# Performance work log

Measured on AMD Instinct MI355X. Metric: run time of the kernel, lower is better.

The kernel has to match this reference:

```python
import jax, jax.numpy as jnp
import numpy as np

B, N, DIM = 8, 1024, 768
HEADS, HEAD_DIM = 8, 96
EXPERTS, TASKS = 24, 9
SCALE = HEAD_DIM ** -0.5
SWITCHLOSS_W, ZLOSS_W = 0.1, 0.001


def setup_inputs() -> dict:
    key = jax.random.key(0)
    ks = jax.random.split(key, 6)
    x = jax.random.normal(ks[0], (B, N, DIM), jnp.float32)
    Wg = jax.random.normal(ks[1], (TASKS, DIM, EXPERTS), jnp.float32) * 0.02  # per-task gate
    W1 = jax.random.normal(ks[2], (EXPERTS, DIM, HEAD_DIM), jnp.float32) * 0.02  # experts (map)
    W2 = jax.random.normal(ks[3], (EXPERTS, HEAD_DIM, DIM), jnp.float32) * 0.02  # output_experts (reduce)
    Wkv = jax.random.normal(ks[4], (DIM, 2 * HEAD_DIM), jnp.float32) * 0.02      # shared kv proj
    b_kv = jax.random.normal(ks[5], (2 * HEAD_DIM,), jnp.float32) * 0.02
    return {"x": x, "Wg\u200b".replace("\u200b", ""): Wg, "W1": W1, "W2": W2, "Wkv": Wkv, "b_kv": b_kv, "task_bh": 3}


def reference(x, Wg, W1, W2, Wkv, b_kv, task_bh):
    # ---- TaskMoE top-k gating (eval mode: clean logits, no noise/sampling) ----
    logits = jnp.einsum('bnd,de->bne', x, Wg[task_bh])            # [B,N,E]
    probs = jax.nn.softmax(logits, axis=-1)
    top_g, top_i = jax.lax.top_k(probs, HEADS)                    # [B,N,H]
    denom = jax.lax.stop_gradient(jnp.sum(top_g, -1, keepdims=True) + 1e-6)
    gates = top_g / denom                                         # normalized top-k gates

    # ---- aux losses: switch (load-balance) + z-loss (cvloss weight is 0) ----
    me = probs.reshape(-1, EXPERTS).sum(0)
    me = me / me.sum()
    freqs = jnp.zeros((EXPERTS,), x.dtype).at[top_i.reshape(-1)].add(1.0)
    fe = freqs / freqs.sum()
    switch_loss = EXPERTS * jnp.sum(me * fe)
    z_loss = jnp.mean(jax.nn.logsumexp(logits.reshape(-1, EXPERTS), axis=-1) ** 2)
    aux_loss = SWITCHLOSS_W * switch_loss + ZLOSS_W * z_loss

    # ---- MoE map: per-head q from selected experts (dense compute + gather) ----
    all_q = jnp.einsum('bnd,edh->bneh', x, W1)                    # [B,N,E,Hd]
    q = jnp.take_along_axis(all_q, top_i[..., None], axis=2)      # [B,N,H,Hd]

    # ---- shared-KV multi-head attention ----
    kv = x @ Wkv + b_kv
    k, v = jnp.split(kv, 2, axis=-1)                              # [B,N,Hd] each
    attn = jnp.einsum('bihd,bjd->bhij', q, k) * SCALE             # [B,H,N,N]
    attn = jax.nn.softmax(attn, axis=-1)
    o = jnp.einsum('bhij,bjd->bihd', attn, v)                     # [B,N,H,Hd]

    # ---- MoE reduce: gate-weighted combine through output experts ----
    comb = jax.nn.one_hot(top_i, EXPERTS, dtype=x.dtype) * gates[..., None]  # [B,N,H,E]
    mixed = jnp.einsum('bnhe,bnhd->bned', comb, o)                # [B,N,E,Hd]
    out = jnp.einsum('bned,edc->bnc', mixed, W2)                  # [B,N,DIM]
    return out, aux_loss
```

## Files before the change

kernel.cpp:

```cpp
#include <hip/hip_runtime.h>
#include <hip/hip_bf16.h>
#include <stdint.h>

#define DEVFN static __device__ __forceinline__

typedef __attribute__((ext_vector_type(8))) short bf16x8;
typedef __attribute__((ext_vector_type(4))) short s16x4;
typedef __attribute__((ext_vector_type(4))) float f32x4;

static constexpr int TOK = 8192;
static constexpr int DIM = 768;
static constexpr int HEADS = 8;
static constexpr int HD = 96;
static constexpr int EXPERTS = 24;
static constexpr int NQ = 2304;
static constexpr int NQP = 2560;
static constexpr float C2 = 0.14724484f;
static constexpr float THRRAW = 78.0f;

static constexpr size_t OFF_XB   = 0;
static constexpr size_t OFF_BT1  = 12582912;
static constexpr size_t OFF_W2T  = 16515072;
static constexpr size_t OFF_K    = 20054016;
static constexpr size_t OFF_VT   = 21626880;
static constexpr size_t OFF_GATE = 23199744;
static constexpr size_t OFF_TOPI = 23461888;
static constexpr size_t OFF_AUX  = 23724032;
static constexpr size_t OFF_ALLQ = 23724288;
static constexpr size_t OFF_PART = OFF_ALLQ;
static constexpr size_t OFF_LOGT = OFF_ALLQ + 6291456;

DEVFN short f2bf(float f){
  __hip_bfloat16 h = __float2bfloat16(f);
  return __builtin_bit_cast(short, h);
}
DEVFN float bf2f(short u){
  return __bfloat162float(__builtin_bit_cast(__hip_bfloat16, u));
}

DEVFN void gload16(const void* g, void* l){
  auto gp = reinterpret_cast<__attribute__((address_space(1))) unsigned int*>(
      reinterpret_cast<uintptr_t>(g));
  auto lp = reinterpret_cast<__attribute__((address_space(3))) unsigned int*>(
      reinterpret_cast<uintptr_t>(l));
  __builtin_amdgcn_global_load_lds(gp, lp, 16, 0, 0);
}

__global__ __launch_bounds__(256) void prep_kernel(const float* __restrict__ W1,
                                                   const float* __restrict__ Wkv,
                                                   const float* __restrict__ W2,
                                                   short* __restrict__ Bt1,
                                                   short* __restrict__ W2t){
  int bid = blockIdx.x, tid = threadIdx.x;
  if (bid < 6912){
    int i = bid*256 + tid;
    int e = i / (DIM*HD);
    int rem = i - e*(DIM*HD);
    int d = rem / HD, hh = rem - d*HD;
    Bt1[(size_t)(e*HD + hh)*DIM + d] = f2bf(W1[i]);
  } else if (bid < 7488){
    int i = (bid-6912)*256 + tid;
    int d = i / 192, j = i - d*192;
    Bt1[(size_t)(NQ + j)*DIM + d] = f2bf(Wkv[i]);
  } else if (bid < 7680){
    int i = (bid-7488)*256 + tid;
    Bt1[(size_t)(NQ + 192)*DIM + i] = 0;
  } else {
    int i = (bid-7680)*256 + tid;
    int e = i / (HD*DIM);
    int rem = i - e*(HD*DIM);
    int hh = rem / DIM, c = rem - hh*DIM;
    W2t[(size_t)c*NQ + e*HD + hh] = f2bf(W2[i]);
  }
}

__global__ __launch_bounds__(64) void gating_partial(const float* __restrict__ x,
                                                     const float* __restrict__ Wg,
                                                     const int* __restrict__ task,
                                                     short* __restrict__ xb,
                                                     float* __restrict__ partial){
  __shared__ float xl[64*101];
  int lane = threadIdx.x;
  int tg = blockIdx.x >> 3, kc = blockIdx.x & 7;
  int tok0 = tg*64, kbase = kc*96;
  const float* Wt = Wg + (size_t)task[0]*(DIM*EXPERTS) + (size_t)kbase*EXPERTS;

#pragma unroll
  for (int i = 0; i < 24; ++i){
    int c = i*64 + lane;
    int t = c / 24, cc = c - t*24;
    size_t gidx = (size_t)(tok0+t)*DIM + kbase + cc*4;
    float4 v = *reinterpret_cast<const float4*>(x + gidx);
    float* dst = &xl[t*101 + cc*4];
    dst[0] = v.x; dst[1] = v.y; dst[2] = v.z; dst[3] = v.w;
    s16x4 o4;
    o4[0] = f2bf(v.x); o4[1] = f2bf(v.y); o4[2] = f2bf(v.z); o4[3] = f2bf(v.w);
    *reinterpret_cast<s16x4*>(xb + gidx) = o4;
  }
  __syncthreads();

  float acc[EXPERTS];
#pragma unroll
  for (int e = 0; e < EXPERTS; ++e) acc[e] = 0.f;
  for (int d = 0; d < 96; ++d){
    float xv = xl[lane*101 + d];
    const float* wr = Wt + d*EXPERTS;
#pragma unroll
    for (int e = 0; e < EXPERTS; ++e) acc[e] = fmaf(xv, wr[e], acc[e]);
  }
#pragma unroll
  for (int e = 0; e < EXPERTS; ++e)
    partial[(size_t)(kc*EXPERTS + e)*TOK + tok0 + lane] = acc[e];
}

__global__ __launch_bounds__(256) void gating_combine(const float* __restrict__ partial,
                                                      float* __restrict__ logT){
  int idx = blockIdx.x*256 + threadIdx.x;
  float s = 0.f;
#pragma unroll
  for (int kc = 0; kc < 8; ++kc)
    s += partial[(size_t)kc*EXPERTS*TOK + idx];
  logT[idx] = s;
}

__global__ __launch_bounds__(256) void gating_select(const float* __restrict__ logT,
                                                     int* __restrict__ topi,
                                                     float* __restrict__ gates,
                                                     float* __restrict__ auxbuf){
  __shared__ float lme[EXPERTS];
  __shared__ float lfr[EXPERTS];
  __shared__ float lz;
  int tid = threadIdx.x;
  int lane = tid & 63;
  int token = blockIdx.x*256 + tid;
  if (tid < EXPERTS){ lme[tid] = 0.f; lfr[tid] = 0.f; }
  if (tid == 0) lz = 0.f;
  __syncthreads();

  float acc[EXPERTS];
#pragma unroll
  for (int e = 0; e < EXPERTS; ++e)
    acc[e] = logT[(size_t)e*TOK + token];

  float mx = acc[0];
#pragma unroll
  for (int e = 1; e < EXPERTS; ++e) mx = fmaxf(mx, acc[e]);
  unsigned selm = 0; int sel[8]; float sg[8];
#pragma unroll
  for (int t = 0; t < 8; ++t){
    float best = -3.0e38f; int bi = 0;
#pragma unroll
    for (int e = 0; e < EXPERTS; ++e){
      bool ok = !((selm>>e)&1u) && (acc[e] > best);
      best = ok ? acc[e] : best;
      bi   = ok ? e      : bi;
    }
    selm |= (1u<<bi); sel[t] = bi; sg[t] = best;
  }

  float p[EXPERTS]; float S = 0.f;
#pragma unroll
  for (int e = 0; e < EXPERTS; ++e){ p[e] = __expf(acc[e] - mx); S += p[e]; }
  float lse = mx + __logf(S);
  float Sinv = 1.f/S;
  float gsum = 0.f; float pg[8];
#pragma unroll
  for (int t = 0; t < 8; ++t){ pg[t] = __expf(sg[t] - mx)*Sinv; gsum += pg[t]; }
  float dinv = 1.f/(gsum + 1e-6f);

#pragma unroll
  for (int t = 0; t < 8; ++t){
    topi[token*HEADS + t]  = sel[t];
    gates[token*HEADS + t] = pg[t]*dinv;
  }

  float z2 = lse*lse;
#pragma unroll
  for (int d = 1; d < 64; d <<= 1) z2 += __shfl_xor(z2, d, 64);
#pragma unroll
  for (int e = 0; e < EXPERTS; ++e){
    float v = p[e]*Sinv;
#pragma unroll
    for (int d = 1; d < 64; d <<= 1) v += __shfl_xor(v, d, 64);
    bool hit = (sel[0]==e)|(sel[1]==e)|(sel[2]==e)|(sel[3]==e)|
               (sel[4]==e)|(sel[5]==e)|(sel[6]==e)|(sel[7]==e);
    unsigned long long bal = __ballot(hit);
    if (lane == 0){
      atomicAdd(&lme[e], v);
      atomicAdd(&lfr[e], (float)__popcll(bal));
    }
  }
  if (lane == 0) atomicAdd(&lz, z2);
  __syncthreads();
  if (tid < EXPERTS){
    atomicAdd(&auxbuf[tid], lme[tid]);
    atomicAdd(&auxbuf[EXPERTS + tid], lfr[tid]);
  } else if (tid == 63) atomicAdd(&auxbuf[2*EXPERTS], lz);
}

__global__ void aux_final(const float* __restrict__ auxbuf, float* __restrict__ outa){
  if (threadIdx.x != 0 || blockIdx.x != 0) return;
  float ms = 0.f, fs = 0.f;
  for (int e=0;e<EXPERTS;++e){ ms += auxbuf[e]; fs += auxbuf[EXPERTS+e]; }
  float sw = 0.f;
  for (int e=0;e<EXPERTS;++e) sw += (auxbuf[e]/ms)*(auxbuf[EXPERTS+e]/fs);
  sw *= (float)EXPERTS;
  float z = auxbuf[2*EXPERTS] / (float)TOK;
  outa[0] = 0.1f*sw + 0.001f*z;
}

template<bool OUT_BF16>
__global__ __launch_bounds__(256) void gemm_bt(const short* __restrict__ A,
                                               const short* __restrict__ Bt,
                                               void* __restrict__ Cout,
                                               int M, int N, int K){
  __shared__ short As[128*64];
  __shared__ short Bs[128*64];
  int nwg = gridDim.x*gridDim.y;
  int orig = blockIdx.y*gridDim.x + blockIdx.x;
  int cpx = nwg >> 3;
  int swz = (orig & 7)*cpx + (orig >> 3);
  int bx = swz % gridDim.x, by = swz / gridDim.x;

  int tid = threadIdx.x;
  int lane = tid & 63, w = tid >> 6;
  int wr = w >> 1, wc = w & 1;
  int l15 = lane & 15, lg = lane >> 4;
  int m0 = by * 128, n0 = bx * 128;

  f32x4 acc[4][4] = {};

  for (int k0 = 0; k0 < K; k0 += 64){
#pragma unroll
    for (int it = 0; it < 4; ++it){
      int c = it*256 + tid;
      int row = c >> 3, cc = c & 7;
      int csrc = cc ^ (row & 7);
      gload16(A  + (size_t)(m0+row)*K + k0 + csrc*8, (char*)As + (size_t)c*16);
      gload16(Bt + (size_t)(n0+row)*K + k0 + csrc*8, (char*)Bs + (size_t)c*16);
    }
    __syncthreads();
#pragma unroll
    for (int kk = 0; kk < 2; ++kk){
      bf16x8 af[4], bfr[4];
      int jp = (kk*4 + lg) ^ (l15 & 7);
#pragma unroll
      for (int m = 0; m < 4; ++m)
        af[m] = *reinterpret_cast<const bf16x8*>(&As[(wr*64 + m*16 + l15)*64 + jp*8]);
#pragma unroll
      for (int n = 0; n < 4; ++n)
        bfr[n] = *reinterpret_cast<const bf16x8*>(&Bs[(wc*64 + n*16 + l15)*64 + jp*8]);
#pragma unroll
      for (int m = 0; m < 4; ++m)
#pragma unroll
        for (int n = 0; n < 4; ++n)
          acc[m][n] = __builtin_amdgcn_mfma_f32_16x16x32_bf16(af[m], bfr[n], acc[m][n], 0, 0, 0);
    }
    __syncthreads();
  }
#pragma unroll
  for (int m = 0; m < 4; ++m)
#pragma unroll
    for (int n = 0; n < 4; ++n){
      int rbase = m0 + wr*64 + m*16 + lg*4;
      int col   = n0 + wc*64 + n*16 + l15;
#pragma unroll
      for (int r = 0; r < 4; ++r){
        float v = acc[m][n][r];
        size_t idx = (size_t)(rbase + r)*N + col;
        if constexpr (OUT_BF16) ((short*)Cout)[idx] = f2bf(v);
        else                    ((float*)Cout)[idx] = v;
      }
    }
}

__global__ __launch_bounds__(256) void gemm2_fused(const short* __restrict__ o,
                                                   const int* __restrict__ topi,
                                                   const short* __restrict__ W2t,
                                                   float* __restrict__ out){
  __shared__ short As[2][128*64];
  __shared__ short Bs[2][64*64];
  __shared__ signed char hmap[128][24];
  int nwg = gridDim.x*gridDim.y;
  int orig = blockIdx.y*gridDim.x + blockIdx.x;
  int cpx = nwg >> 3;
  int swz = (orig & 7)*cpx + (orig >> 3);
  int bx = swz % gridDim.x, by = swz / gridDim.x;

  int tid = threadIdx.x;
  int lane = tid & 63, w = tid >> 6;
  int l15 = lane & 15, lg = lane >> 4;
  int m0 = by * 128, n0 = bx * 64;

  int* hm32 = (int*)&hmap[0][0];
  for (int i = tid; i < 768; i += 256) hm32[i] = -1;
  __syncthreads();
  for (int i = tid; i < 128*8; i += 256){
    int row = i >> 3, hh = i & 7;
    int e = topi[(size_t)(m0+row)*HEADS + hh];
    hmap[row][e] = (signed char)hh;
  }
  __syncthreads();

  int arow[4], accv[4];
  size_t arbase[4];
#pragma unroll
  for (int it = 0; it < 4; ++it){
    int c = it*256 + tid;
    arow[it] = c >> 3; accv[it] = c & 7;
    arbase[it] = (size_t)(m0 + arow[it])*DIM;
  }

  f32x4 acc[2][4] = {};
  bf16x8 areg[4];

#define STAGE_A(kt, dst)                                                     \
  {                                                                          \
    _Pragma("unroll")                                                        \
    for (int it = 0; it < 4; ++it){                                          \
      unsigned kc = (unsigned)((kt)*8 + accv[it]);                           \
      unsigned e = kc / 12u;                                                 \
      unsigned dc = kc - e*12u;                                              \
      int hh = hmap[arow[it]][e];                                            \
      bf16x8 av = {};                                                        \
      if (hh >= 0)                                                           \
        av = *reinterpret_cast<const bf16x8*>(o + arbase[it] + hh*HD + dc*8);\
      dst[it] = av;                                                          \
    }                                                                        \
  }
#define WRITE_A(buf, src)                                                    \
  {                                                                          \
    _Pragma("unroll")                                                        \
    for (int it = 0; it < 4; ++it)                                           \
      *reinterpret_cast<bf16x8*>(                                            \
        &As[buf][arow[it]*64 + ((accv[it] ^ (arow[it] & 7)))*8]) = src[it];  \
  }
#define STAGE_B(kt, buf)                                                     \
  {                                                                          \
    _Pragma("unroll")                                                        \
    for (int it = 0; it < 2; ++it){                                          \
      int c = it*256 + tid;                                                  \
      int row = c >> 3, cc = c & 7;                                          \
      int csrc = cc ^ (row & 7);                                             \
      gload16(W2t + (size_t)(n0+row)*NQ + (kt)*64 + csrc*8,                  \
              (char*)&Bs[buf][0] + (size_t)c*16);                            \
    }                                                                        \
  }

  STAGE_A(0, areg);
  STAGE_B(0, 0);
  WRITE_A(0, areg);
  __syncthreads();

  for (int kt = 0; kt < 36; ++kt){
    int buf = kt & 1;
    bf16x8 anext[4];
    if (kt < 35){
      STAGE_A(kt+1, anext);
      STAGE_B(kt+1, buf^1);
    }
#pragma unroll
    for (int kk = 0; kk < 2; ++kk){
      int jp = (kk*4 + lg) ^ (l15 & 7);
      bf16x8 af[2], bfr[4];
#pragma unroll
      for (int m = 0; m < 2; ++m)
        af[m] = *reinterpret_cast<const bf16x8*>(&As[buf][(w*32 + m*16 + l15)*64 + jp*8]);
#pragma unroll
      for (int n = 0; n < 4; ++n)
        bfr[n] = *reinterpret_cast<const bf16x8*>(&Bs[buf][(n*16 + l15)*64 + jp*8]);
#pragma unroll
      for (int m = 0; m < 2; ++m)
#pragma unroll
        for (int n = 0; n < 4; ++n)
          acc[m][n] = __builtin_amdgcn_mfma_f32_16x16x32_bf16(af[m], bfr[n], acc[m][n], 0, 0, 0);
    }
    if (kt < 35) WRITE_A(buf^1, anext);
    __syncthreads();
  }
#undef STAGE_A
#undef WRITE_A
#undef STAGE_B

#pragma unroll
  for (int m = 0; m < 2; ++m)
#pragma unroll
    for (int n = 0; n < 4; ++n){
      int rbase = m0 + w*32 + m*16 + lg*4;
      int col   = n0 + n*16 + l15;
#pragma unroll
      for (int r = 0; r < 4; ++r)
        out[(size_t)(rbase + r)*DIM + col] = acc[m][n][r];
    }
}

__global__ __launch_bounds__(256) void split_kv_tile(const short* __restrict__ allq,
                                                     const float* __restrict__ bkv,
                                                     short* __restrict__ Kp,
                                                     short* __restrict__ Vp){
  __shared__ short kv[64*192];
  int bt = blockIdx.x;
  int b = bt >> 4;
  int tid = threadIdx.x;
#pragma unroll
  for (int it = 0; it < 6; ++it){
    int c = it*256 + tid;
    int j = c / 24, cc = c - j*24;
    int token = b*1024 + (bt & 15)*64 + j;
    gload16(allq + (size_t)token*NQP + NQ + cc*8, (char*)kv + (size_t)c*16);
  }
  __syncthreads();
#pragma unroll
  for (int it = 0; it < 3; ++it){
    int c = it*256 + tid;
    int kc = c >> 6, j = c & 63;
    bf16x8 v = *reinterpret_cast<const bf16x8*>(&kv[j*192 + kc*8]);
    bf16x8 o8;
#pragma unroll
    for (int e = 0; e < 8; ++e) o8[e] = f2bf(bf2f(v[e]) + bkv[kc*8 + e]);
    *reinterpret_cast<bf16x8*>(Kp + ((size_t)bt*768 + c)*8) = o8;
  }
#pragma unroll
  for (int it = 0; it < 3; ++it){
    int c = it*256 + tid;
    int kc = c / 96, hd = c - kc*96;
    float bias = bkv[96 + hd];
    bf16x8 o8;
#pragma unroll
    for (int e = 0; e < 8; ++e) o8[e] = f2bf(bf2f(kv[(kc*8 + e)*192 + 96 + hd]) + bias);
    *reinterpret_cast<bf16x8*>(Vp + ((size_t)bt*768 + c)*8) = o8;
  }
}

__global__ __launch_bounds__(256, 2) void attn_fwd(const short* __restrict__ allq,
                                                   const int* __restrict__ topi,
                                                   const float* __restrict__ gates,
                                                   const short* __restrict__ Kp,
                                                   const short* __restrict__ Vp,
                                                   short* __restrict__ o){
  __shared__ short Klds[2][768*8];
  __shared__ short Vlds[2][768*8];
  __shared__ short Plds[4][16*72];
  int qt = blockIdx.x, bh = blockIdx.y;
  int b = bh >> 3, h = bh & 7;
  int tid = threadIdx.x;
  int lane = tid & 63, w = tid >> 6;
  int l15 = lane & 15, lg = lane >> 4;

  bf16x8 qf[2][3];
  int tok0 = b*1024 + qt*128 + w*32;
#pragma unroll
  for (int qm = 0; qm < 2; ++qm){
    int token = tok0 + qm*16 + l15;
    int qe = topi[token*HEADS + h];
    const short* qp = allq + (size_t)token*NQP + qe*HD;
#pragma unroll
    for (int t = 0; t < 3; ++t)
      qf[qm][t] = *reinterpret_cast<const bf16x8*>(qp + t*32 + lg*8);
  }

  f32x4 Oacc[2][6] = {};
  float mrun[2][4], lrun[2][4];
#pragma unroll
  for (int qm = 0; qm < 2; ++qm)
#pragma unroll
    for (int r = 0; r < 4; ++r){ mrun[qm][r] = -1.0e30f; lrun[qm][r] = 0.f; }

  const short* kb = Kp + (size_t)b*16*768*8;
  const short* vb = Vp + (size_t)b*16*768*8;

#pragma unroll
  for (int it = 0; it < 3; ++it){
    int c = it*256 + tid;
    gload16(kb + (size_t)c*8, (char*)&Klds[0][0] + (size_t)c*16);
    gload16(vb + (size_t)c*8, (char*)&Vlds[0][0] + (size_t)c*16);
  }
  __syncthreads();

  int cur = 0;
  for (int nt = 0; nt < 16; ++nt){
    if (nt < 15){
      const short* kn = kb + (size_t)(nt+1)*768*8;
      const short* vn = vb + (size_t)(nt+1)*768*8;
#pragma unroll
      for (int it = 0; it < 3; ++it){
        int c = it*256 + tid;
        gload16(kn + (size_t)c*8, (char*)&Klds[cur^1][0] + (size_t)c*16);
        gload16(vn + (size_t)c*8, (char*)&Vlds[cur^1][0] + (size_t)c*16);
      }
    }

    f32x4 sa[2][4];
    __builtin_amdgcn_s_setprio(1);
#pragma unroll
    for (int ct = 0; ct < 4; ++ct){
      bf16x8 kf[3];
#pragma unroll
      for (int t = 0; t < 3; ++t)
        kf[t] = *reinterpret_cast<const bf16x8*>(&Klds[cur][((t*4+lg)*64 + ct*16 + l15)*8]);
#pragma unroll
      for (int qm = 0; qm < 2; ++qm){
        f32x4 a = {};
#pragma unroll
        for (int t = 0; t < 3; ++t)
          a = __builtin_amdgcn_mfma_f32_16x16x32_bf16(qf[qm][t], kf[t], a, 0, 0, 0);
        sa[qm][ct] = a;
      }
    }
    __builtin_amdgcn_s_setprio(0);

    float pmax[2][4];
    bool need = false;
#pragma unroll
    for (int qm = 0; qm < 2; ++qm)
#pragma unroll
      for (int r = 0; r < 4; ++r){
        pmax[qm][r] = fmaxf(fmaxf(sa[qm][0][r], sa[qm][1][r]),
                            fmaxf(sa[qm][2][r], sa[qm][3][r]));
        need = need || (pmax[qm][r] > mrun[qm][r] + THRRAW);
      }
    if (__any(need)){
#pragma unroll
      for (int qm = 0; qm < 2; ++qm)
#pragma unroll
        for (int r = 0; r < 4; ++r){
          float mx = pmax[qm][r];
#pragma unroll
          for (int d = 1; d < 16; d <<= 1) mx = fmaxf(mx, __shfl_xor(mx, d, 64));
          float mnew = fmaxf(mrun[qm][r], mx);
          float al = exp2f((mrun[qm][r] - mnew)*C2);
          lrun[qm][r] *= al;
#pragma unroll
          for (int dt = 0; dt < 6; ++dt) Oacc[qm][dt][r] *= al;
          mrun[qm][r] = mnew;
        }
    }

#pragma unroll
    for (int qm = 0; qm < 2; ++qm)
#pragma unroll
      for (int r = 0; r < 4; ++r){
        float mc = mrun[qm][r]*C2;
        float s = 0.f;
#pragma unroll
        for (int ct = 0; ct < 4; ++ct){
          float p = exp2f(fmaf(sa[qm][ct][r], C2, -mc));
          sa[qm][ct][r] = p; s += p;
        }
        lrun[qm][r] += s;
      }

    bf16x8 vf[2][6];
#pragma unroll
    for (int ct = 0; ct < 4; ++ct)
#pragma unroll
      for (int r = 0; r < 4; ++r)
        Plds[w][(lg*4 + r)*72 + ct*16 + l15] = f2bf(sa[0][ct][r]);
    __builtin_amdgcn_s_setprio(1);
#pragma unroll
    for (int ks = 0; ks < 2; ++ks){
      bf16x8 pa = *reinterpret_cast<const bf16x8*>(&Plds[w][l15*72 + ks*32 + lg*8]);
#pragma unroll
      for (int dt = 0; dt < 6; ++dt){
        vf[ks][dt] = *reinterpret_cast<const bf16x8*>(&Vlds[cur][((ks*4+lg)*96 + dt*16 + l15)*8]);
        Oacc[0][dt] = __builtin_amdgcn_mfma_f32_16x16x32_bf16(pa, vf[ks][dt], Oacc[0][dt], 0, 0, 0);
      }
    }
    __builtin_amdgcn_s_setprio(0);
#pragma unroll
    for (int ct = 0; ct < 4; ++ct)
#pragma unroll
      for (int r = 0; r < 4; ++r)
        Plds[w][(lg*4 + r)*72 + ct*16 + l15] = f2bf(sa[1][ct][r]);
    __builtin_amdgcn_s_setprio(1);
#pragma unroll
    for (int ks = 0; ks < 2; ++ks){
      bf16x8 pa = *reinterpret_cast<const bf16x8*>(&Plds[w][l15*72 + ks*32 + lg*8]);
#pragma unroll
      for (int dt = 0; dt < 6; ++dt)
        Oacc[1][dt] = __builtin_amdgcn_mfma_f32_16x16x32_bf16(pa, vf[ks][dt], Oacc[1][dt], 0, 0, 0);
    }
    __builtin_amdgcn_s_setprio(0);

    __syncthreads();
    cur ^= 1;
  }

#pragma unroll
  for (int qm = 0; qm < 2; ++qm)
#pragma unroll
    for (int r = 0; r < 4; ++r){
      float l = lrun[qm][r];
#pragma unroll
      for (int d = 1; d < 16; d <<= 1) l += __shfl_xor(l, d, 64);
      int token = tok0 + qm*16 + lg*4 + r;
      float inv = gates[token*HEADS + h] / l;
#pragma unroll
      for (int dt = 0; dt < 6; ++dt)
        o[(size_t)token*DIM + h*HD + dt*16 + l15] = f2bf(Oacc[qm][dt][r]*inv);
    }
}

extern "C" void kernel_launch(void* const* d_in, const int* in_sizes, int n_in,
                              void* d_out, int out_size, void* d_ws, size_t ws_size,
                              hipStream_t stream) {
  (void)in_sizes; (void)n_in; (void)out_size; (void)ws_size;
  const float* x    = (const float*)d_in[0];
  const float* Wg   = (const float*)d_in[1];
  const float* W1   = (const float*)d_in[2];
  const float* W2   = (const float*)d_in[3];
  const float* Wkv  = (const float*)d_in[4];
  const float* bkv  = (const float*)d_in[5];
  const int*   task = (const int*)d_in[6];

  char* ws = (char*)d_ws;
  short* xb    = (short*)(ws + OFF_XB);
  short* o     = (short*)(ws + OFF_XB);
  short* Bt1   = (short*)(ws + OFF_BT1);
  short* W2t   = (short*)(ws + OFF_W2T);
  short* Kp    = (short*)(ws + OFF_K);
  short* Vp    = (short*)(ws + OFF_VT);
  float* gates = (float*)(ws + OFF_GATE);
  int*   topi  = (int*)(ws + OFF_TOPI);
  float* aux   = (float*)(ws + OFF_AUX);
  short* allq  = (short*)(ws + OFF_ALLQ);
  float* part  = (float*)(ws + OFF_PART);
  float* logT  = (float*)(ws + OFF_LOGT);
  float* out   = (float*)d_out;

  hipMemsetAsync(aux, 0, 256, stream);
  prep_kernel   <<<14592, 256, 0, stream>>>(W1, Wkv, W2, Bt1, W2t);
  gating_partial<<<1024, 64, 0, stream>>>(x, Wg, task, xb, part);
  gating_combine<<<768, 256, 0, stream>>>(part, logT);
  gating_select <<<32, 256, 0, stream>>>(logT, topi, gates, aux);
  aux_final     <<<1, 64, 0, stream>>>(aux, out + (size_t)TOK*DIM);
  gemm_bt<true><<<dim3(NQP/128, TOK/128), 256, 0, stream>>>(xb, Bt1, allq, TOK, NQP, DIM);
  split_kv_tile<<<128, 256, 0, stream>>>(allq, bkv, Kp, Vp);
  attn_fwd     <<<dim3(8, 64), 256, 0, stream>>>(allq, topi, gates, Kp, Vp, o);
  gemm2_fused  <<<dim3(DIM/64, TOK/128), 256, 0, stream>>>(o, topi, W2t, out);
}
```

Measured before the change: 203.9 us.

## Tile weight transposes through LDS and split gating reduction into more chunks

```diff
diff --git a/kernel.cpp b/kernel.cpp
--- a/kernel.cpp
+++ b/kernel.cpp
@@ -28,7 +28,7 @@
 static constexpr size_t OFF_AUX  = 23724032;
 static constexpr size_t OFF_ALLQ = 23724288;
 static constexpr size_t OFF_PART = OFF_ALLQ;
-static constexpr size_t OFF_LOGT = OFF_ALLQ + 6291456;
+static constexpr size_t OFF_LOGT = OFF_ALLQ + 12582912;
 
 DEVFN short f2bf(float f){
   __hip_bfloat16 h = __float2bfloat16(f);
@@ -51,26 +51,79 @@
                                                    const float* __restrict__ W2,
                                                    short* __restrict__ Bt1,
                                                    short* __restrict__ W2t){
+  __shared__ float tl[6240];
   int bid = blockIdx.x, tid = threadIdx.x;
-  if (bid < 6912){
-    int i = bid*256 + tid;
-    int e = i / (DIM*HD);
-    int rem = i - e*(DIM*HD);
-    int d = rem / HD, hh = rem - d*HD;
-    Bt1[(size_t)(e*HD + hh)*DIM + d] = f2bf(W1[i]);
-  } else if (bid < 7488){
-    int i = (bid-6912)*256 + tid;
-    int d = i / 192, j = i - d*192;
-    Bt1[(size_t)(NQ + j)*DIM + d] = f2bf(Wkv[i]);
-  } else if (bid < 7680){
-    int i = (bid-7488)*256 + tid;
+
+  if (bid < 288){
+    int e = bid / 12, dt = bid - e*12;
+    int d0 = dt*64;
+    const float* src = W1 + (size_t)e*(DIM*HD);
+#pragma unroll
+    for (int it = 0; it < 6; ++it){
+      int c = it*256 + tid;
+      int row = c / 24, q = c - row*24;
+      float4 v = *reinterpret_cast<const float4*>(src + (size_t)(d0+row)*HD + q*4);
+      float* dst = &tl[row*97 + q*4];
+      dst[0]=v.x; dst[1]=v.y; dst[2]=v.z; dst[3]=v.w;
+    }
+    __syncthreads();
+#pragma unroll
+    for (int it = 0; it < 6; ++it){
+      int c = it*256 + tid;
+      int hh = c >> 4, cq = c & 15;
+      s16x4 o4;
+#pragma unroll
+      for (int j = 0; j < 4; ++j) o4[j] = f2bf(tl[(cq*4+j)*97 + hh]);
+      *reinterpret_cast<s16x4*>(Bt1 + (size_t)(e*HD + hh)*DIM + d0 + cq*4) = o4;
+    }
+  } else if (bid < 312){
+    int t = bid - 288;
+    int jb = t / 12, dt = t - jb*12;
+    int j0 = jb*96, d0 = dt*64;
+#pragma unroll
+    for (int it = 0; it < 6; ++it){
+      int c = it*256 + tid;
+      int row = c / 24, q = c - row*24;
+      float4 v = *reinterpret_cast<const float4*>(Wkv + (size_t)(d0+row)*192 + j0 + q*4);
+      float* dst = &tl[row*97 + q*4];
+      dst[0]=v.x; dst[1]=v.y; dst[2]=v.z; dst[3]=v.w;
+    }
+    __syncthreads();
+#pragma unroll
+    for (int it = 0; it < 6; ++it){
+      int c = it*256 + tid;
+      int jj = c >> 4, cq = c & 15;
+      s16x4 o4;
+#pragma unroll
+      for (int j = 0; j < 4; ++j) o4[j] = f2bf(tl[(cq*4+j)*97 + jj]);
+      *reinterpret_cast<s16x4*>(Bt1 + (size_t)(NQ + j0 + jj)*DIM + d0 + cq*4) = o4;
+    }
+  } else if (bid < 600){
+    int t = bid - 312;
+    int e = t / 12, ct = t - e*12;
+    int c0 = ct*64;
+    const float* src = W2 + (size_t)e*(HD*DIM);
+#pragma unroll
+    for (int it = 0; it < 6; ++it){
+      int c = it*256 + tid;
+      int hh = c >> 4, q = c & 15;
+      float4 v = *reinterpret_cast<const float4*>(src + (size_t)hh*DIM + c0 + q*4);
+      float* dst = &tl[hh*65 + q*4];
+      dst[0]=v.x; dst[1]=v.y; dst[2]=v.z; dst[3]=v.w;
+    }
+    __syncthreads();
+#pragma unroll
+    for (int it = 0; it < 6; ++it){
+      int c = it*256 + tid;
+      int cr = c / 24, q = c - cr*24;
+      s16x4 o4;
+#pragma unroll
+      for (int j = 0; j < 4; ++j) o4[j] = f2bf(tl[(q*4+j)*65 + cr]);
+      *reinterpret_cast<s16x4*>(W2t + (size_t)(c0 + cr)*NQ + e*HD + q*4) = o4;
+    }
+  } else {
+    int i = (bid-600)*256 + tid;
     Bt1[(size_t)(NQ + 192)*DIM + i] = 0;
-  } else {
-    int i = (bid-7680)*256 + tid;
-    int e = i / (HD*DIM);
-    int rem = i - e*(HD*DIM);
-    int hh = rem / DIM, c = rem - hh*DIM;
-    W2t[(size_t)c*NQ + e*HD + hh] = f2bf(W2[i]);
   }
 }
 
@@ -79,19 +132,19 @@
                                                      const int* __restrict__ task,
                                                      short* __restrict__ xb,
                                                      float* __restrict__ partial){
-  __shared__ float xl[64*101];
+  __shared__ float xl[64*49];
   int lane = threadIdx.x;
-  int tg = blockIdx.x >> 3, kc = blockIdx.x & 7;
-  int tok0 = tg*64, kbase = kc*96;
+  int tg = blockIdx.x >> 4, kc = blockIdx.x & 15;
+  int tok0 = tg*64, kbase = kc*48;
   const float* Wt = Wg + (size_t)task[0]*(DIM*EXPERTS) + (size_t)kbase*EXPERTS;
 
 #pragma unroll
-  for (int i = 0; i < 24; ++i){
+  for (int i = 0; i < 12; ++i){
     int c = i*64 + lane;
-    int t = c / 24, cc = c - t*24;
+    int t = c / 12, cc = c - t*12;
     size_t gidx = (size_t)(tok0+t)*DIM + kbase + cc*4;
     float4 v = *reinterpret_cast<const float4*>(x + gidx);
-    float* dst = &xl[t*101 + cc*4];
+    float* dst = &xl[t*49 + cc*4];
     dst[0] = v.x; dst[1] = v.y; dst[2] = v.z; dst[3] = v.w;
     s16x4 o4;
     o4[0] = f2bf(v.x); o4[1] = f2bf(v.y); o4[2] = f2bf(v.z); o4[3] = f2bf(v.w);
@@ -102,8 +155,8 @@
   float acc[EXPERTS];
 #pragma unroll
   for (int e = 0; e < EXPERTS; ++e) acc[e] = 0.f;
-  for (int d = 0; d < 96; ++d){
-    float xv = xl[lane*101 + d];
+  for (int d = 0; d < 48; ++d){
+    float xv = xl[lane*49 + d];
     const float* wr = Wt + d*EXPERTS;
 #pragma unroll
     for (int e = 0; e < EXPERTS; ++e) acc[e] = fmaf(xv, wr[e], acc[e]);
@@ -118,7 +171,7 @@
   int idx = blockIdx.x*256 + threadIdx.x;
   float s = 0.f;
 #pragma unroll
-  for (int kc = 0; kc < 8; ++kc)
+  for (int kc = 0; kc < 16; ++kc)
     s += partial[(size_t)kc*EXPERTS*TOK + idx];
   logT[idx] = s;
 }
@@ -629,8 +682,8 @@
   float* out   = (float*)d_out;
 
   hipMemsetAsync(aux, 0, 256, stream);
-  prep_kernel   <<<14592, 256, 0, stream>>>(W1, Wkv, W2, Bt1, W2t);
-  gating_partial<<<1024, 64, 0, stream>>>(x, Wg, task, xb, part);
+  prep_kernel   <<<792, 256, 0, stream>>>(W1, Wkv, W2, Bt1, W2t);
+  gating_partial<<<2048, 64, 0, stream>>>(x, Wg, task, xb, part);
   gating_combine<<<768, 256, 0, stream>>>(part, logT);
   gating_select <<<32, 256, 0, stream>>>(logT, topi, gates, aux);
   aux_final     <<<1, 64, 0, stream>>>(aux, out + (size_t)TOK*DIM);
```

Result: faster. 187.6 us (-8.0%).
